# Optimization experiments

Measured on AMD Instinct MI355X. Metric: run time of the kernel, lower is better.

Reference implementation:

```python
import jax, jax.numpy as jnp
import numpy as np

N = 100000
E = 1600000
NUM_GRAPHS = 64
EPS = 1e-5


def setup_inputs() -> dict:
    key = jax.random.key(0)
    ks = jax.random.split(key, 8)
    x = jax.random.normal(ks[0], (N, 128), dtype=jnp.float32)
    edge_index = jax.random.randint(ks[1], (2, E), 0, N, dtype=jnp.int64)
    batch = jnp.sort(jax.random.randint(ks[2], (N,), 0, NUM_GRAPHS, dtype=jnp.int64))
    W1 = jax.random.normal(ks[3], (128, 128), dtype=jnp.float32) * (1.0 / np.sqrt(128))
    W2 = jax.random.normal(ks[4], (128, 128), dtype=jnp.float32) * (1.0 / np.sqrt(128))
    W3 = jax.random.normal(ks[5], (128, 32), dtype=jnp.float32) * (1.0 / np.sqrt(128))
    return {
        'x': x, 'edge_index': edge_index, 'batch': batch,
        'W1': W1, 'b1': jnp.zeros((128,), jnp.float32),
        'W2': W2, 'b2': jnp.zeros((128,), jnp.float32),
        'W3': W3, 'b3': jnp.zeros((32,), jnp.float32),
        'gamma1': jnp.ones((128,), jnp.float32), 'beta1': jnp.zeros((128,), jnp.float32),
        'gamma2': jnp.ones((128,), jnp.float32), 'beta2': jnp.zeros((128,), jnp.float32),
    }


def _gcn_norm(edge_index, n_nodes):
    # PyG GCNConv default: add self-loops, symmetric normalization.
    loop = jnp.arange(n_nodes, dtype=edge_index.dtype)
    src = jnp.concatenate([edge_index[0], loop])  # [E+N]
    dst = jnp.concatenate([edge_index[1], loop])
    deg = jax.ops.segment_sum(jnp.ones_like(dst, dtype=jnp.float32), dst,
                              num_segments=n_nodes)
    dinv = jnp.where(deg > 0, jax.lax.rsqrt(deg), 0.0)
    norm = dinv[src] * dinv[dst]  # [E+N]
    return src, dst, norm


def _gcn_conv(x, W, b, src, dst, norm, n_nodes):
    h = x @ W                                   # [N, d_out] dense GEMM
    msg = h[src] * norm[:, None]                # gather + scale  [E+N, d_out]
    out = jax.ops.segment_sum(msg, dst, num_segments=n_nodes)  # scatter-add
    return out + b


def _batchnorm(x, gamma, beta):
    # Training-mode BatchNorm1d: batch stats over node dim, biased variance.
    mean = jnp.mean(x, axis=0)
    var = jnp.var(x, axis=0)
    return (x - mean) * jax.lax.rsqrt(var + EPS) * gamma + beta


def reference(x, edge_index, batch, W1, b1, W2, b2, W3, b3,
              gamma1, beta1, gamma2, beta2):
    src, dst, norm = _gcn_norm(edge_index, N)
    h = _gcn_conv(x, W1, b1, src, dst, norm, N)
    h = jax.nn.relu(_batchnorm(h, gamma1, beta1))  # dropout is identity (eval)
    h = _gcn_conv(h, W2, b2, src, dst, norm, N)
    h = jax.nn.relu(_batchnorm(h, gamma2, beta2))
    h = _gcn_conv(h, W3, b3, src, dst, norm, N)
    # global_mean_pool over graph ids
    sums = jax.ops.segment_sum(h, batch, num_segments=NUM_GRAPHS)  # [G, out]
    cnts = jax.ops.segment_sum(jnp.ones((N,), jnp.float32), batch,
                               num_segments=NUM_GRAPHS)
    pooled = sums / jnp.maximum(cnts, 1.0)[:, None]
    return jax.nn.sigmoid(pooled)
```

## Files before the change

### kernel.cpp

```cpp
#include <hip/hip_runtime.h>
#include <math.h>

#define NGRAPH 64
#define EPS_BN 1e-5f
#define BN_BLOCKS 512

typedef unsigned int uint32;
typedef unsigned short ushort16;
typedef __attribute__((ext_vector_type(8))) short short8v;
typedef __attribute__((ext_vector_type(4))) float float4v;

__device__ __forceinline__ float bf2f(uint32 u16) {
    return __uint_as_float(u16 << 16);
}
__device__ __forceinline__ ushort16 f2bf(float f) {
    uint32 u = __float_as_uint(f);
    return (ushort16)((u + 0x7fffu + ((u >> 16) & 1u)) >> 16);
}
__device__ __forceinline__ uint32 pack2(float lo, float hi) {
    return (uint32)f2bf(lo) | ((uint32)f2bf(hi) << 16);
}

__global__ __launch_bounds__(256) void k_cnt_r(const int* __restrict__ dst,
                                               int* __restrict__ cnt,
                                               int* __restrict__ rank, int ne) {
    int i = blockIdx.x * 256 + threadIdx.x;
    if (i < ne) rank[i] = atomicAdd(&cnt[dst[i]], 1);
}

__global__ __launch_bounds__(1024) void k_scan1(const int* __restrict__ cnt,
                                                int* __restrict__ rowstart,
                                                int* __restrict__ blocksum,
                                                float* __restrict__ dinv, int n) {
    __shared__ int sh[1024];
    const int tid = threadIdx.x;
    const int i = blockIdx.x * 1024 + tid;
    int v = (i < n) ? cnt[i] : 0;
    if (i < n) dinv[i] = rsqrtf((float)(v + 1));
    sh[tid] = v;
    __syncthreads();
    for (int off = 1; off < 1024; off <<= 1) {
        int t = (tid >= off) ? sh[tid - off] : 0;
        __syncthreads();
        sh[tid] += t;
        __syncthreads();
    }
    if (i < n) rowstart[i] = sh[tid] - v;
    if (tid == 1023) blocksum[blockIdx.x] = sh[1023];
}

__global__ __launch_bounds__(1024) void k_scan2(int* __restrict__ blocksum, int nb,
                                                float* __restrict__ psum,
                                                float* __restrict__ pcnt) {
    __shared__ int sh[1024];
    const int tid = threadIdx.x;
    int v = (tid < nb) ? blocksum[tid] : 0;
    sh[tid] = v;
    __syncthreads();
    for (int off = 1; off < 1024; off <<= 1) {
        int t = (tid >= off) ? sh[tid - off] : 0;
        __syncthreads();
        sh[tid] += t;
        __syncthreads();
    }
    if (tid < nb) blocksum[tid] = sh[tid] - v;
    for (int i = tid; i < NGRAPH * 32; i += 1024) psum[i] = 0.f;
    if (tid < NGRAPH) pcnt[tid] = 0.f;
}

__global__ __launch_bounds__(256) void k_scan3(int* __restrict__ rowstart,
                                               const int* __restrict__ blocksum, int n) {
    int i = blockIdx.x * 256 + threadIdx.x;
    if (i < n) rowstart[i] += blocksum[i >> 10];
}

__global__ __launch_bounds__(256) void k_scatter_nr(const int* __restrict__ src,
                                                    const int* __restrict__ dst,
                                                    const int* __restrict__ rank,
                                                    const int* __restrict__ rowstart,
                                                    int* __restrict__ esrc, int ne) {
    int i = blockIdx.x * 256 + threadIdx.x;
    if (i < ne) esrc[rowstart[dst[i]] + rank[i]] = src[i];
}

__global__ __launch_bounds__(256) void k_wprep_all(const float* __restrict__ W1,
                                                   const float* __restrict__ W2,
                                                   const float* __restrict__ W3,
                                                   ushort16* __restrict__ wt1,
                                                   ushort16* __restrict__ wt2,
                                                   ushort16* __restrict__ wt3,
                                                   int* __restrict__ cnt, int n) {
    int i = blockIdx.x * 256 + threadIdx.x;
    if (i < 16384) {
        int c = i >> 7, k = i & 127;
        wt1[i] = f2bf(W1[k * 128 + c]);
    } else if (i < 32768) {
        int j = i - 16384;
        int c = j >> 7, k = j & 127;
        wt2[j] = f2bf(W2[k * 128 + c]);
    } else if (i < 36864) {
        int j = i - 32768;
        int c = j >> 7, k = j & 127;
        wt3[j] = f2bf(W3[k * 32 + c]);
    }
    if (i < n) cnt[i] = 0;
}

template<int COLS, bool BN, bool AF32>
__global__ __launch_bounds__(256) void k_gemm_mfma(const void* __restrict__ Av,
                                                   const ushort16* __restrict__ Wt,
                                                   const float* __restrict__ ss,
                                                   const float* __restrict__ dinv,
                                                   ushort16* __restrict__ C, int nrows) {
    constexpr int K = 128;
    constexpr int LDK = K + 8;
    __shared__ ushort16 As[64 * LDK];
    __shared__ ushort16 Bs[COLS * LDK];
    const int tid = threadIdx.x;

    {
        const uint4* wg = (const uint4*)Wt;
        for (int i = tid; i < COLS * (K / 8); i += 256) {
            int r = i >> 4, c8 = i & 15;
            *(uint4*)&Bs[r * LDK + c8 * 8] = wg[i];
        }
    }

    const int w = tid >> 6;
    const int l = tid & 63;
    const int lr = l & 15;
    const int lg = l >> 4;
    constexpr int CT = COLS / 16;

    #pragma unroll
    for (int half = 0; half < 2; ++half) {
        const int row0 = blockIdx.x * 128 + half * 64;
        if (half) __syncthreads();
        if constexpr (AF32) {
            const float* A = (const float*)Av;
            for (int i = tid; i < 64 * (K / 4); i += 256) {
                int r = i >> 5, c4 = i & 31;
                float4 a;
                if (row0 + r < nrows) a = *(const float4*)&A[(size_t)(row0 + r) * K + c4 * 4];
                else a = make_float4(0.f, 0.f, 0.f, 0.f);
                if (BN) {
                    float4 sc = *(const float4*)&ss[c4 * 4];
                    float4 sh = *(const float4*)&ss[128 + c4 * 4];
                    a.x = fmaxf(fmaf(a.x, sc.x, sh.x), 0.f);
                    a.y = fmaxf(fmaf(a.y, sc.y, sh.y), 0.f);
                    a.z = fmaxf(fmaf(a.z, sc.z, sh.z), 0.f);
                    a.w = fmaxf(fmaf(a.w, sc.w, sh.w), 0.f);
                }
                ushort4 o;
                o.x = f2bf(a.x); o.y = f2bf(a.y); o.z = f2bf(a.z); o.w = f2bf(a.w);
                *(ushort4*)&As[r * LDK + c4 * 4] = o;
            }
        } else {
            const uint4* Ag = (const uint4*)Av;
            for (int i = tid; i < 64 * (K / 8); i += 256) {
                int r = i >> 4, c8 = i & 15;
                uint4 u;
                if (row0 + r < nrows) u = Ag[(size_t)(row0 + r) * 16 + c8];
                else u = make_uint4(0, 0, 0, 0);
                if (BN) {
                    uint32 wv[4] = {u.x, u.y, u.z, u.w};
                    #pragma unroll
                    for (int t = 0; t < 4; ++t) {
                        int f = c8 * 8 + t * 2;
                        float lo = fmaxf(fmaf(bf2f(wv[t] & 0xffffu), ss[f],     ss[128 + f]),     0.f);
                        float hi = fmaxf(fmaf(bf2f(wv[t] >> 16),     ss[f + 1], ss[128 + f + 1]), 0.f);
                        wv[t] = pack2(lo, hi);
                    }
                    u.x = wv[0]; u.y = wv[1]; u.z = wv[2]; u.w = wv[3];
                }
                *(uint4*)&As[r * LDK + c8 * 8] = u;
            }
        }
        __syncthreads();

        float4v acc[CT] = {};
        short8v afrag[4];
        #pragma unroll
        for (int kk = 0; kk < 4; ++kk)
            afrag[kk] = *(const short8v*)&As[(w * 16 + lr) * LDK + kk * 32 + lg * 8];
        #pragma unroll
        for (int kk = 0; kk < 4; ++kk) {
            #pragma unroll
            for (int ct = 0; ct < CT; ++ct) {
                short8v b = *(const short8v*)&Bs[(ct * 16 + lr) * LDK + kk * 32 + lg * 8];
                acc[ct] = __builtin_amdgcn_mfma_f32_16x16x32_bf16(afrag[kk], b, acc[ct], 0, 0, 0);
            }
        }
        #pragma unroll
        for (int r = 0; r < 4; ++r) {
            int gr = row0 + w * 16 + lg * 4 + r;
            if (gr < nrows) {
                float dv = dinv[gr];
                #pragma unroll
                for (int ct = 0; ct < CT; ++ct)
                    C[(size_t)gr * COLS + ct * 16 + lr] = f2bf(acc[ct][r] * dv);
            }
        }
    }
}

template<int COLS>
__global__ __launch_bounds__(256) void k_agg_csr(const ushort16* __restrict__ h,
                                                 const int* __restrict__ rowstart,
                                                 const int* __restrict__ cnt,
                                                 const int* __restrict__ esrc,
                                                 const float* __restrict__ dinv,
                                                 uint32* __restrict__ out, int n) {
    constexpr int TPN = COLS / 2;
    const uint32* __restrict__ hu = (const uint32*)h;
    int gt = blockIdx.x * 256 + threadIdx.x;
    int node = gt / TPN;
    if (node >= n) return;
    int lane = gt % TPN;

    float di = dinv[node];
    uint32 p = hu[(size_t)node * TPN + lane];
    float ax = bf2f(p & 0xffffu);
    float ay = bf2f(p >> 16);

    int beg = rowstart[node];
    int dg = cnt[node];
    if constexpr (TPN == 64) {
        beg = __builtin_amdgcn_readfirstlane(beg);
        dg = __builtin_amdgcn_readfirstlane(dg);
    }
    const int end = beg + dg;
    int e = beg;
    for (; e + 4 <= end; e += 4) {
        int s0 = esrc[e], s1 = esrc[e + 1], s2 = esrc[e + 2], s3 = esrc[e + 3];
        uint32 p0 = hu[(size_t)s0 * TPN + lane];
        uint32 p1 = hu[(size_t)s1 * TPN + lane];
        uint32 p2 = hu[(size_t)s2 * TPN + lane];
        uint32 p3 = hu[(size_t)s3 * TPN + lane];
        ax += bf2f(p0 & 0xffffu); ay += bf2f(p0 >> 16);
        ax += bf2f(p1 & 0xffffu); ay += bf2f(p1 >> 16);
        ax += bf2f(p2 & 0xffffu); ay += bf2f(p2 >> 16);
        ax += bf2f(p3 & 0xffffu); ay += bf2f(p3 >> 16);
    }
    for (; e < end; ++e) {
        int s0 = esrc[e];
        uint32 p0 = hu[(size_t)s0 * TPN + lane];
        ax += bf2f(p0 & 0xffffu);
        ay += bf2f(p0 >> 16);
    }
    out[(size_t)node * TPN + lane] = pack2(ax * di, ay * di);
}

__global__ __launch_bounds__(256) void k_bn_stats1(const uint32* __restrict__ x,
                                                   float* __restrict__ partials, int n) {
    const int cp = threadIdx.x & 63;
    const int rl = threadIdx.x >> 6;
    float s0 = 0.f, s1 = 0.f, q0 = 0.f, q1 = 0.f;
    for (int r = blockIdx.x * 4 + rl; r < n; r += BN_BLOCKS * 4) {
        uint32 u = x[(size_t)r * 64 + cp];
        float lo = bf2f(u & 0xffffu), hi = bf2f(u >> 16);
        s0 += lo; s1 += hi;
        q0 = fmaf(lo, lo, q0); q1 = fmaf(hi, hi, q1);
    }
    __shared__ float shs[4 * 128];
    __shared__ float shq[4 * 128];
    shs[rl * 128 + 2 * cp] = s0; shs[rl * 128 + 2 * cp + 1] = s1;
    shq[rl * 128 + 2 * cp] = q0; shq[rl * 128 + 2 * cp + 1] = q1;
    __syncthreads();
    int f = threadIdx.x;
    if (f < 128) {
        float s = shs[f] + shs[128 + f] + shs[256 + f] + shs[384 + f];
        float q = shq[f] + shq[128 + f] + shq[256 + f] + shq[384 + f];
        partials[(size_t)blockIdx.x * 256 + f] = s;
        partials[(size_t)blockIdx.x * 256 + 128 + f] = q;
    }
}

__global__ __launch_bounds__(256) void k_bn_stats2(const float* __restrict__ partials,
                                                   const float* __restrict__ gamma,
                                                   const float* __restrict__ beta,
                                                   float* __restrict__ ss, int n) {
    const int f16 = threadIdx.x & 15;
    const int rl = threadIdx.x >> 4;
    const int f = blockIdx.x * 16 + f16;
    float s = 0.f, q = 0.f;
    for (int r = rl; r < BN_BLOCKS; r += 16) {
        s += partials[(size_t)r * 256 + f];
        q += partials[(size_t)r * 256 + 128 + f];
    }
    __shared__ float shs[256], shq[256];
    shs[threadIdx.x] = s;
    shq[threadIdx.x] = q;
    __syncthreads();
    if (rl == 0) {
        float S = 0.f, Q = 0.f;
        #pragma unroll
        for (int r = 0; r < 16; ++r) { S += shs[r * 16 + f16]; Q += shq[r * 16 + f16]; }
        float inv_n = 1.0f / (float)n;
        float mean = S * inv_n;
        float var = Q * inv_n - mean * mean;
        float scale = gamma[f] * rsqrtf(var + EPS_BN);
        ss[f] = scale;
        ss[128 + f] = beta[f] - mean * scale;
    }
}

#define POOL_SLICE 128
__global__ __launch_bounds__(256) void k_pool2(const uint32* __restrict__ h3,
                                               const int* __restrict__ batch,
                                               float* __restrict__ sums,
                                               float* __restrict__ cnt, int n) {
    const int fp = threadIdx.x & 15;
    const int sub = threadIdx.x >> 4;
    int node0 = blockIdx.x * (16 * POOL_SLICE) + sub * POOL_SLICE;
    if (node0 >= n) return;
    int node1 = min(node0 + POOL_SLICE, n);

    int cur_g = batch[node0];
    float a0 = 0.f, a1 = 0.f, c = 0.f;
    for (int i = node0; i < node1; ++i) {
        int g = batch[i];
        if (g != cur_g) {
            atomicAdd(&sums[cur_g * 32 + 2 * fp], a0);
            atomicAdd(&sums[cur_g * 32 + 2 * fp + 1], a1);
            if (fp == 0) atomicAdd(&cnt[cur_g], c);
            a0 = 0.f; a1 = 0.f; c = 0.f; cur_g = g;
        }
        uint32 u = h3[(size_t)i * 16 + fp];
        a0 += bf2f(u & 0xffffu);
        a1 += bf2f(u >> 16);
        c += 1.f;
    }
    atomicAdd(&sums[cur_g * 32 + 2 * fp], a0);
    atomicAdd(&sums[cur_g * 32 + 2 * fp + 1], a1);
    if (fp == 0) atomicAdd(&cnt[cur_g], c);
}

__global__ __launch_bounds__(256) void k_final(const float* __restrict__ sums,
                                               const float* __restrict__ cnt,
                                               const float* __restrict__ b3,
                                               float* __restrict__ out) {
    int i = blockIdx.x * 256 + threadIdx.x;
    if (i >= NGRAPH * 32) return;
    int g = i >> 5;
    int f = i & 31;
    float c = fmaxf(cnt[g], 1.0f);
    float v = sums[i] / c + b3[f];
    out[i] = 1.0f / (1.0f + expf(-v));
}

extern "C" void kernel_launch(void* const* d_in, const int* in_sizes, int n_in,
                              void* d_out, int out_size, void* d_ws, size_t ws_size,
                              hipStream_t stream) {
    const float* x      = (const float*)d_in[0];
    const int*   eidx   = (const int*)d_in[1];
    const int*   batch  = (const int*)d_in[2];
    const float* W1     = (const float*)d_in[3];
    const float* W2     = (const float*)d_in[5];
    const float* W3     = (const float*)d_in[7];
    const float* b3     = (const float*)d_in[8];
    const float* gamma1 = (const float*)d_in[9];
    const float* beta1  = (const float*)d_in[10];
    const float* gamma2 = (const float*)d_in[11];
    const float* beta2  = (const float*)d_in[12];

    const int N = in_sizes[0] / 128;
    const int E = in_sizes[1] / 2;
    const int* src = eidx;
    const int* dst = eidx + E;

    size_t off = 0;
    auto carve = [&](size_t bytes) {
        char* p = (char*)d_ws + off;
        off += (bytes + 511) & ~(size_t)511;
        return p;
    };
    const size_t NB = (size_t)N * 128 * sizeof(float);
    ushort16* bufA  = (ushort16*)carve(NB / 2);
    uint32* bufB    = (uint32*)carve(NB / 2);
    int*   cnt      = (int*)carve((size_t)N * 4);
    int*   rowstart = (int*)carve((size_t)N * 4);
    float* dinv     = (float*)carve((size_t)N * 4);
    int*   esrc     = (int*)carve((size_t)E * 4);
    int*   rank     = (int*)carve((size_t)E * 4);
    ushort16* wt1   = (ushort16*)carve(128 * 128 * 2);
    ushort16* wt2   = (ushort16*)carve(128 * 128 * 2);
    ushort16* wt3   = (ushort16*)carve(32 * 128 * 2);
    float* ss1      = (float*)carve(256 * 4);
    float* ss2      = (float*)carve(256 * 4);
    float* partials = (float*)carve((size_t)BN_BLOCKS * 256 * 4);
    int*   blocksum = (int*)carve(1024 * 4);
    float* psum     = (float*)carve(NGRAPH * 32 * 4);
    float* pcnt     = (float*)carve(NGRAPH * 4);
    (void)ws_size; (void)n_in; (void)out_size;

    const int nblkN   = (N + 255) / 256;
    const int nblkE   = (E + 255) / 256;
    const int nbScan  = (N + 1023) / 1024;
    const int nbGemm  = (N + 127) / 128;
    const int nblkAgg128 = ((size_t)N * 64 + 255) / 256;
    const int nblkAgg32  = ((size_t)N * 16 + 255) / 256;
    const int nblkPool   = (N + 16 * POOL_SLICE - 1) / (16 * POOL_SLICE);
    const int nbWprep    = (((36864 > N) ? 36864 : N) + 255) / 256;

    k_wprep_all<<<nbWprep, 256, 0, stream>>>(W1, W2, W3, wt1, wt2, wt3, cnt, N);

    k_cnt_r<<<nblkE, 256, 0, stream>>>(dst, cnt, rank, E);
    k_scan1<<<nbScan, 1024, 0, stream>>>(cnt, rowstart, blocksum, dinv, N);
    k_scan2<<<1, 1024, 0, stream>>>(blocksum, nbScan, psum, pcnt);
    k_scan3<<<nblkN, 256, 0, stream>>>(rowstart, blocksum, N);
    k_scatter_nr<<<nblkE, 256, 0, stream>>>(src, dst, rank, rowstart, esrc, E);

    k_gemm_mfma<128, false, true><<<nbGemm, 256, 0, stream>>>(x, wt1, nullptr, dinv, bufA, N);
    k_agg_csr<128><<<nblkAgg128, 256, 0, stream>>>(bufA, rowstart, cnt, esrc, dinv, bufB, N);
    k_bn_stats1<<<BN_BLOCKS, 256, 0, stream>>>(bufB, partials, N);
    k_bn_stats2<<<8, 256, 0, stream>>>(partials, gamma1, beta1, ss1, N);

    k_gemm_mfma<128, true, false><<<nbGemm, 256, 0, stream>>>(bufB, wt2, ss1, dinv, bufA, N);
    k_agg_csr<128><<<nblkAgg128, 256, 0, stream>>>(bufA, rowstart, cnt, esrc, dinv, bufB, N);
    k_bn_stats1<<<BN_BLOCKS, 256, 0, stream>>>(bufB, partials, N);
    k_bn_stats2<<<8, 256, 0, stream>>>(partials, gamma2, beta2, ss2, N);

    k_gemm_mfma<32, true, false><<<nbGemm, 256, 0, stream>>>(bufB, wt3, ss2, dinv, bufA, N);
    k_agg_csr<32><<<nblkAgg32, 256, 0, stream>>>(bufA, rowstart, cnt, esrc, dinv, bufB, N);

    k_pool2<<<nblkPool, 256, 0, stream>>>(bufB, batch, psum, pcnt, N);
    k_final<<<(NGRAPH * 32 + 255) / 256, 256, 0, stream>>>(psum, pcnt, b3, (float*)d_out);
}
```

Measured before the change: 411.3 us.

## Fuse first GEMM with degree counting and merge scan3 into edge scatter

The first-layer GEMM no longer depends on dinv, so it now runs in the same launch as the atomic in-degree counting: every fourth block in the first 4*EB slots counts edges while the rest do GEMM tiles. The scan3 offset fixup is folded into the CSR scatter kernel, which adds blocksum on the fly and writes a separate final rowstart array. Because the first aggregation now sees unscaled features, it multiplies each neighbour by dinv[src], adding an extra gather per edge in that pass. The aim is fewer launches and overlapping the atomic counting with the GEMM, at the cost of more per-edge work in layer one.

```diff
diff --git a/kernel.cpp b/kernel.cpp
--- a/kernel.cpp
+++ b/kernel.cpp
@@ -19,68 +19,6 @@
 }
 __device__ __forceinline__ uint32 pack2(float lo, float hi) {
     return (uint32)f2bf(lo) | ((uint32)f2bf(hi) << 16);
-}
-
-__global__ __launch_bounds__(256) void k_cnt_r(const int* __restrict__ dst,
-                                               int* __restrict__ cnt,
-                                               int* __restrict__ rank, int ne) {
-    int i = blockIdx.x * 256 + threadIdx.x;
-    if (i < ne) rank[i] = atomicAdd(&cnt[dst[i]], 1);
-}
-
-__global__ __launch_bounds__(1024) void k_scan1(const int* __restrict__ cnt,
-                                                int* __restrict__ rowstart,
-                                                int* __restrict__ blocksum,
-                                                float* __restrict__ dinv, int n) {
-    __shared__ int sh[1024];
-    const int tid = threadIdx.x;
-    const int i = blockIdx.x * 1024 + tid;
-    int v = (i < n) ? cnt[i] : 0;
-    if (i < n) dinv[i] = rsqrtf((float)(v + 1));
-    sh[tid] = v;
-    __syncthreads();
-    for (int off = 1; off < 1024; off <<= 1) {
-        int t = (tid >= off) ? sh[tid - off] : 0;
-        __syncthreads();
-        sh[tid] += t;
-        __syncthreads();
-    }
-    if (i < n) rowstart[i] = sh[tid] - v;
-    if (tid == 1023) blocksum[blockIdx.x] = sh[1023];
-}
-
-__global__ __launch_bounds__(1024) void k_scan2(int* __restrict__ blocksum, int nb,
-                                                float* __restrict__ psum,
-                                                float* __restrict__ pcnt) {
-    __shared__ int sh[1024];
-    const int tid = threadIdx.x;
-    int v = (tid < nb) ? blocksum[tid] : 0;
-    sh[tid] = v;
-    __syncthreads();
-    for (int off = 1; off < 1024; off <<= 1) {
-        int t = (tid >= off) ? sh[tid - off] : 0;
-        __syncthreads();
-        sh[tid] += t;
-        __syncthreads();
-    }
-    if (tid < nb) blocksum[tid] = sh[tid] - v;
-    for (int i = tid; i < NGRAPH * 32; i += 1024) psum[i] = 0.f;
-    if (tid < NGRAPH) pcnt[tid] = 0.f;
-}
-
-__global__ __launch_bounds__(256) void k_scan3(int* __restrict__ rowstart,
-                                               const int* __restrict__ blocksum, int n) {
-    int i = blockIdx.x * 256 + threadIdx.x;
-    if (i < n) rowstart[i] += blocksum[i >> 10];
-}
-
-__global__ __launch_bounds__(256) void k_scatter_nr(const int* __restrict__ src,
-                                                    const int* __restrict__ dst,
-                                                    const int* __restrict__ rank,
-                                                    const int* __restrict__ rowstart,
-                                                    int* __restrict__ esrc, int ne) {
-    int i = blockIdx.x * 256 + threadIdx.x;
-    if (i < ne) esrc[rowstart[dst[i]] + rank[i]] = src[i];
 }
 
 __global__ __launch_bounds__(256) void k_wprep_all(const float* __restrict__ W1,
@@ -104,6 +42,156 @@
         wt3[j] = f2bf(W3[k * 32 + c]);
     }
     if (i < n) cnt[i] = 0;
+}
+
+#define EB 256
+__global__ __launch_bounds__(256) void k_gemm1_cnt(const float* __restrict__ A,
+                                                   const ushort16* __restrict__ Wt,
+                                                   ushort16* __restrict__ C, int nrows,
+                                                   const int* __restrict__ dst,
+                                                   int* __restrict__ cnt,
+                                                   int* __restrict__ rank,
+                                                   int ne, int epb) {
+    constexpr int K = 128;
+    constexpr int COLS = 128;
+    constexpr int LDK = K + 8;
+    __shared__ ushort16 As[64 * LDK];
+    __shared__ ushort16 Bs[COLS * LDK];
+    const int tid = threadIdx.x;
+    const int bid = blockIdx.x;
+    const int q = bid >> 2, r = bid & 3;
+
+    if (r == 3 && q < EB) {
+        const int beg = q * epb;
+        const int end = min(beg + epb, ne);
+        int e = beg + tid;
+        for (; e + 3 * 256 < end; e += 4 * 256) {
+            int d0 = dst[e], d1 = dst[e + 256], d2 = dst[e + 512], d3 = dst[e + 768];
+            int r0 = atomicAdd(&cnt[d0], 1);
+            int r1 = atomicAdd(&cnt[d1], 1);
+            int r2 = atomicAdd(&cnt[d2], 1);
+            int r3 = atomicAdd(&cnt[d3], 1);
+            rank[e] = r0; rank[e + 256] = r1; rank[e + 512] = r2; rank[e + 768] = r3;
+        }
+        for (; e < end; e += 256) rank[e] = atomicAdd(&cnt[dst[e]], 1);
+        return;
+    }
+    const int gidx = (q < EB) ? (3 * q + r) : (bid - EB);
+
+    {
+        const uint4* wg = (const uint4*)Wt;
+        for (int i = tid; i < COLS * (K / 8); i += 256) {
+            int rr = i >> 4, c8 = i & 15;
+            *(uint4*)&Bs[rr * LDK + c8 * 8] = wg[i];
+        }
+    }
+    const int w = tid >> 6;
+    const int l = tid & 63;
+    const int lr = l & 15;
+    const int lg = l >> 4;
+    constexpr int CT = COLS / 16;
+
+    #pragma unroll
+    for (int half = 0; half < 2; ++half) {
+        const int row0 = gidx * 128 + half * 64;
+        if (half) __syncthreads();
+        const float* Af = A;
+        for (int i = tid; i < 64 * (K / 4); i += 256) {
+            int rr = i >> 5, c4 = i & 31;
+            float4 a;
+            if (row0 + rr < nrows) a = *(const float4*)&Af[(size_t)(row0 + rr) * K + c4 * 4];
+            else a = make_float4(0.f, 0.f, 0.f, 0.f);
+            ushort4 o;
+            o.x = f2bf(a.x); o.y = f2bf(a.y); o.z = f2bf(a.z); o.w = f2bf(a.w);
+            *(ushort4*)&As[rr * LDK + c4 * 4] = o;
+        }
+        __syncthreads();
+
+        float4v acc[CT] = {};
+        short8v afrag[4];
+        #pragma unroll
+        for (int kk = 0; kk < 4; ++kk)
+            afrag[kk] = *(const short8v*)&As[(w * 16 + lr) * LDK + kk * 32 + lg * 8];
+        #pragma unroll
+        for (int kk = 0; kk < 4; ++kk) {
+            #pragma unroll
+            for (int ct = 0; ct < CT; ++ct) {
+                short8v b = *(const short8v*)&Bs[(ct * 16 + lr) * LDK + kk * 32 + lg * 8];
+                acc[ct] = __builtin_amdgcn_mfma_f32_16x16x32_bf16(afrag[kk], b, acc[ct], 0, 0, 0);
+            }
+        }
+        #pragma unroll
+        for (int rr = 0; rr < 4; ++rr) {
+            int gr = row0 + w * 16 + lg * 4 + rr;
+            if (gr < nrows) {
+                #pragma unroll
+                for (int ct = 0; ct < CT; ++ct)
+                    C[(size_t)gr * COLS + ct * 16 + lr] = f2bf(acc[ct][rr]);
+            }
+        }
+    }
+}
+
+__global__ __launch_bounds__(1024) void k_scan1(const int* __restrict__ cnt,
+                                                int* __restrict__ rowstart,
+                                                int* __restrict__ blocksum,
+                                                float* __restrict__ dinv, int n) {
+    __shared__ int sh[1024];
+    const int tid = threadIdx.x;
+    const int i = blockIdx.x * 1024 + tid;
+    int v = (i < n) ? cnt[i] : 0;
+    if (i < n) dinv[i] = rsqrtf((float)(v + 1));
+    sh[tid] = v;
+    __syncthreads();
+    for (int off = 1; off < 1024; off <<= 1) {
+        int t = (tid >= off) ? sh[tid - off] : 0;
+        __syncthreads();
+        sh[tid] += t;
+        __syncthreads();
+    }
+    if (i < n) rowstart[i] = sh[tid] - v;
+    if (tid == 1023) blocksum[blockIdx.x] = sh[1023];
+}
+
+__global__ __launch_bounds__(1024) void k_scan2(int* __restrict__ blocksum, int nb,
+                                                float* __restrict__ psum,
+                                                float* __restrict__ pcnt) {
+    __shared__ int sh[1024];
+    const int tid = threadIdx.x;
+    int v = (tid < nb) ? blocksum[tid] : 0;
+    sh[tid] = v;
+    __syncthreads();
+    for (int off = 1; off < 1024; off <<= 1) {
+        int t = (tid >= off) ? sh[tid - off] : 0;
+        __syncthreads();
+        sh[tid] += t;
+        __syncthreads();
+    }
+    if (tid < nb) blocksum[tid] = sh[tid] - v;
+    for (int i = tid; i < NGRAPH * 32; i += 1024) psum[i] = 0.f;
+    if (tid < NGRAPH) pcnt[tid] = 0.f;
+}
+
+__global__ __launch_bounds__(256) void k_scan3s(const int* __restrict__ src,
+                                                const int* __restrict__ dst,
+                                                const int* __restrict__ rank,
+                                                const int* __restrict__ rowstart,
+                                                const int* __restrict__ blocksum,
+                                                int* __restrict__ rowfin,
+                                                int* __restrict__ esrc, int n, int ne) {
+    const int tid = threadIdx.x;
+    const int bid = blockIdx.x;
+    int i = bid * 256 + tid;
+    if (i < n) rowfin[i] = rowstart[i] + blocksum[i >> 10];
+    int e0 = bid * 2048 + tid;
+    #pragma unroll
+    for (int j = 0; j < 8; ++j) {
+        int e = e0 + j * 256;
+        if (e < ne) {
+            int d = dst[e];
+            esrc[rowstart[d] + blocksum[d >> 10] + rank[e]] = src[e];
+        }
+    }
 }
 
 template<int COLS, bool BN, bool AF32>
@@ -204,7 +292,7 @@
     }
 }
 
-template<int COLS>
+template<int COLS, bool PRESCALED>
 __global__ __launch_bounds__(256) void k_agg_csr(const ushort16* __restrict__ h,
                                                  const int* __restrict__ rowstart,
                                                  const int* __restrict__ cnt,
@@ -220,8 +308,14 @@
 
     float di = dinv[node];
     uint32 p = hu[(size_t)node * TPN + lane];
-    float ax = bf2f(p & 0xffffu);
-    float ay = bf2f(p >> 16);
+    float ax, ay;
+    if constexpr (PRESCALED) {
+        ax = bf2f(p & 0xffffu);
+        ay = bf2f(p >> 16);
+    } else {
+        ax = bf2f(p & 0xffffu) * di;
+        ay = bf2f(p >> 16) * di;
+    }
 
     int beg = rowstart[node];
     int dg = cnt[node];
@@ -237,16 +331,30 @@
         uint32 p1 = hu[(size_t)s1 * TPN + lane];
         uint32 p2 = hu[(size_t)s2 * TPN + lane];
         uint32 p3 = hu[(size_t)s3 * TPN + lane];
-        ax += bf2f(p0 & 0xffffu); ay += bf2f(p0 >> 16);
-        ax += bf2f(p1 & 0xffffu); ay += bf2f(p1 >> 16);
-        ax += bf2f(p2 & 0xffffu); ay += bf2f(p2 >> 16);
-        ax += bf2f(p3 & 0xffffu); ay += bf2f(p3 >> 16);
+        if constexpr (PRESCALED) {
+            ax += bf2f(p0 & 0xffffu); ay += bf2f(p0 >> 16);
+            ax += bf2f(p1 & 0xffffu); ay += bf2f(p1 >> 16);
+            ax += bf2f(p2 & 0xffffu); ay += bf2f(p2 >> 16);
+            ax += bf2f(p3 & 0xffffu); ay += bf2f(p3 >> 16);
+        } else {
+            float w0 = dinv[s0], w1 = dinv[s1], w2 = dinv[s2], w3 = dinv[s3];
+            ax = fmaf(bf2f(p0 & 0xffffu), w0, ax); ay = fmaf(bf2f(p0 >> 16), w0, ay);
+            ax = fmaf(bf2f(p1 & 0xffffu), w1, ax); ay = fmaf(bf2f(p1 >> 16), w1, ay);
+            ax = fmaf(bf2f(p2 & 0xffffu), w2, ax); ay = fmaf(bf2f(p2 >> 16), w2, ay);
+            ax = fmaf(bf2f(p3 & 0xffffu), w3, ax); ay = fmaf(bf2f(p3 >> 16), w3, ay);
+        }
     }
     for (; e < end; ++e) {
         int s0 = esrc[e];
         uint32 p0 = hu[(size_t)s0 * TPN + lane];
-        ax += bf2f(p0 & 0xffffu);
-        ay += bf2f(p0 >> 16);
+        if constexpr (PRESCALED) {
+            ax += bf2f(p0 & 0xffffu);
+            ay += bf2f(p0 >> 16);
+        } else {
+            float w0 = dinv[s0];
+            ax = fmaf(bf2f(p0 & 0xffffu), w0, ax);
+            ay = fmaf(bf2f(p0 >> 16), w0, ay);
+        }
     }
     out[(size_t)node * TPN + lane] = pack2(ax * di, ay * di);
 }
@@ -380,6 +488,7 @@
     uint32* bufB    = (uint32*)carve(NB / 2);
     int*   cnt      = (int*)carve((size_t)N * 4);
     int*   rowstart = (int*)carve((size_t)N * 4);
+    int*   rowfin   = (int*)carve((size_t)N * 4);
     float* dinv     = (float*)carve((size_t)N * 4);
     int*   esrc     = (int*)carve((size_t)E * 4);
     int*   rank     = (int*)carve((size_t)E * 4);
@@ -394,35 +503,35 @@
     float* pcnt     = (float*)carve(NGRAPH * 4);
     (void)ws_size; (void)n_in; (void)out_size;
 
-    const int nblkN   = (N + 255) / 256;
-    const int nblkE   = (E + 255) / 256;
     const int nbScan  = (N + 1023) / 1024;
     const int nbGemm  = (N + 127) / 128;
     const int nblkAgg128 = ((size_t)N * 64 + 255) / 256;
     const int nblkAgg32  = ((size_t)N * 16 + 255) / 256;
     const int nblkPool   = (N + 16 * POOL_SLICE - 1) / (16 * POOL_SLICE);
     const int nbWprep    = (((36864 > N) ? 36864 : N) + 255) / 256;
+    const int nbS3       = (E + 2047) / 2048;
+    const int epb        = (E + EB - 1) / EB;
+    const int nbFused    = nbGemm + EB;
 
     k_wprep_all<<<nbWprep, 256, 0, stream>>>(W1, W2, W3, wt1, wt2, wt3, cnt, N);
 
-    k_cnt_r<<<nblkE, 256, 0, stream>>>(dst, cnt, rank, E);
+    k_gemm1_cnt<<<nbFused, 256, 0, stream>>>(x, wt1, bufA, N, dst, cnt, rank, E, epb);
+
     k_scan1<<<nbScan, 1024, 0, stream>>>(cnt, rowstart, blocksum, dinv, N);
     k_scan2<<<1, 1024, 0, stream>>>(blocksum, nbScan, psum, pcnt);
-    k_scan3<<<nblkN, 256, 0, stream>>>(rowstart, blocksum, N);
-    k_scatter_nr<<<nblkE, 256, 0, stream>>>(src, dst, rank, rowstart, esrc, E);
-
-    k_gemm_mfma<128, false, true><<<nbGemm, 256, 0, stream>>>(x, wt1, nullptr, dinv, bufA, N);
-    k_agg_csr<128><<<nblkAgg128, 256, 0, stream>>>(bufA, rowstart, cnt, esrc, dinv, bufB, N);
+    k_scan3s<<<nbS3, 256, 0, stream>>>(src, dst, rank, rowstart, blocksum, rowfin, esrc, N, E);
+
+    k_agg_csr<128, false><<<nblkAgg128, 256, 0, stream>>>(bufA, rowfin, cnt, esrc, dinv, bufB, N);
     k_bn_stats1<<<BN_BLOCKS, 256, 0, stream>>>(bufB, partials, N);
     k_bn_stats2<<<8, 256, 0, stream>>>(partials, gamma1, beta1, ss1, N);
 
     k_gemm_mfma<128, true, false><<<nbGemm, 256, 0, stream>>>(bufB, wt2, ss1, dinv, bufA, N);
-    k_agg_csr<128><<<nblkAgg128, 256, 0, stream>>>(bufA, rowstart, cnt, esrc, dinv, bufB, N);
+    k_agg_csr<128, true><<<nblkAgg128, 256, 0, stream>>>(bufA, rowfin, cnt, esrc, dinv, bufB, N);
     k_bn_stats1<<<BN_BLOCKS, 256, 0, stream>>>(bufB, partials, N);
     k_bn_stats2<<<8, 256, 0, stream>>>(partials, gamma2, beta2, ss2, N);
 
     k_gemm_mfma<32, true, false><<<nbGemm, 256, 0, stream>>>(bufB, wt3, ss2, dinv, bufA, N);
-    k_agg_csr<32><<<nblkAgg32, 256, 0, stream>>>(bufA, rowstart, cnt, esrc, dinv, bufB, N);
+    k_agg_csr<32, true><<<nblkAgg32, 256, 0, stream>>>(bufA, rowfin, cnt, esrc, dinv, bufB, N);
 
     k_pool2<<<nblkPool, 256, 0, stream>>>(bufB, batch, psum, pcnt, N);
     k_final<<<(NGRAPH * 32 + 255) / 256, 256, 0, stream>>>(psum, pcnt, b3, (float*)d_out);
```

Measured after the change: 398.0 us. 1.03x faster.
